# Kernel optimization log

Measured on AMD Instinct MI355X. Metric: run time of the kernel, lower is better.

## Reference

```python
import jax, jax.numpy as jnp
import numpy as np

HIDDEN = 2048
NUM_HEADS = 16
HEAD_DIM = 128
WINDOW_SIZE = 512
NUM_GLOBAL = 16
SCALING = HEAD_DIM ** -0.5


def setup_inputs() -> dict:
    key = jax.random.key(0)
    ks = jax.random.split(key, 5)
    std = HIDDEN ** -0.5
    hidden_states = jax.random.normal(ks[0], (1, 4096, HIDDEN), dtype=jnp.float32)
    # Linear weights stored as (in, out) so y = x @ W
    Wq = jax.random.normal(ks[1], (HIDDEN, NUM_HEADS * HEAD_DIM), dtype=jnp.float32) * std
    Wk = jax.random.normal(ks[2], (HIDDEN, NUM_HEADS * HEAD_DIM), dtype=jnp.float32) * std
    Wv = jax.random.normal(ks[3], (HIDDEN, NUM_HEADS * HEAD_DIM), dtype=jnp.float32) * std
    Wo = jax.random.normal(ks[4], (NUM_HEADS * HEAD_DIM, HIDDEN), dtype=jnp.float32) * std
    return {"hidden_states": hidden_states, "Wq": Wq, "Wk": Wk, "Wv": Wv, "Wo": Wo}


def _sliding_mask(q_len: int, kv_len: int) -> jnp.ndarray:
    q_pos = jnp.arange(q_len)[:, None]
    kv_pos = jnp.arange(kv_len)[None, :]
    half_window = WINDOW_SIZE // 2
    local = jnp.abs(q_pos - kv_pos) < half_window
    glob = (q_pos < NUM_GLOBAL) | (kv_pos < NUM_GLOBAL)
    mask = local | glob
    return jnp.where(mask, 0.0, -jnp.inf).astype(jnp.float32)


def reference(hidden_states, Wq, Wk, Wv, Wo):
    bsz, q_len, _ = hidden_states.shape
    q = (hidden_states @ Wq).reshape(bsz, q_len, NUM_HEADS, HEAD_DIM).transpose(0, 2, 1, 3)
    k = (hidden_states @ Wk).reshape(bsz, q_len, NUM_HEADS, HEAD_DIM).transpose(0, 2, 1, 3)
    v = (hidden_states @ Wv).reshape(bsz, q_len, NUM_HEADS, HEAD_DIM).transpose(0, 2, 1, 3)
    mask = _sliding_mask(q_len, q_len)[None, None]  # [1,1,S,S]
    scores = jnp.einsum("bhqd,bhkd->bhqk", q, k) * SCALING + mask
    attn = jax.nn.softmax(scores.astype(jnp.float32), axis=-1).astype(q.dtype)
    out = jnp.einsum("bhqk,bhkd->bhqd", attn, v)
    out = out.transpose(0, 2, 1, 3).reshape(bsz, q_len, NUM_HEADS * HEAD_DIM)
    return out @ Wo
```

## Files before the change

### kernel.cpp

```cpp
#include <hip/hip_runtime.h>
#include <stdint.h>

#define SEQ    4096
#define HID    2048
#define NQKV   6144
#define NH     16
#define HD     128
#define SCALE  0.08838834764831845f
#define GQC    32

typedef unsigned short u16;
typedef __attribute__((ext_vector_type(8))) short bf16x8;
typedef __attribute__((ext_vector_type(4))) float f32x4;

__device__ __forceinline__ u16 f2bf(float f) {
  union { float f; unsigned u; } v; v.f = f;
  unsigned r = v.u + 0x7FFFu + ((v.u >> 16) & 1u);
  return (u16)(r >> 16);
}

__device__ __forceinline__ float bf2f(u16 b) {
  union { unsigned u; float f; } c; c.u = ((unsigned)b) << 16; return c.f;
}

__device__ __forceinline__ void async16(const u16* g, u16* l) {
  __builtin_amdgcn_global_load_lds(
      (const __attribute__((address_space(1))) unsigned int*)g,
      (__attribute__((address_space(3))) unsigned int*)l, 16, 0, 0);
}

__global__ __launch_bounds__(256) void cvt_f32_bf16(const float* __restrict__ in,
                                                    u16* __restrict__ out, int n4) {
  int i = blockIdx.x * 256 + threadIdx.x;
  if (i >= n4) return;
  float4 v = ((const float4*)in)[i];
  ushort4 o;
  o.x = f2bf(v.x); o.y = f2bf(v.y); o.z = f2bf(v.z); o.w = f2bf(v.w);
  ((ushort4*)out)[i] = o;
}

__global__ __launch_bounds__(256) void transpose_w(const float* __restrict__ W,
                                                   u16* __restrict__ Wt) {
  __shared__ __align__(16) u16 Ts[64 * 72];
  const int n0 = blockIdx.x * 64;
  const int k0 = blockIdx.y * 64;
  const int t = threadIdx.x;
#pragma unroll
  for (int p = 0; p < 4; ++p) {
    int f = (t + p * 256) * 4;
    int r = f >> 6, c = f & 63;
    float4 v = *(const float4*)&W[(size_t)(k0 + r) * 2048 + n0 + c];
    ushort4 o; o.x = f2bf(v.x); o.y = f2bf(v.y); o.z = f2bf(v.z); o.w = f2bf(v.w);
    *(ushort4*)&Ts[r * 72 + c] = o;
  }
  __syncthreads();
#pragma unroll
  for (int p = 0; p < 4; ++p) {
    int g = (t + p * 256) * 4;
    int r = g >> 6, c = g & 63;
    ushort4 o;
    o.x = Ts[(c + 0) * 72 + r];
    o.y = Ts[(c + 1) * 72 + r];
    o.z = Ts[(c + 2) * 72 + r];
    o.w = Ts[(c + 3) * 72 + r];
    *(ushort4*)&Wt[(size_t)(n0 + r) * 2048 + k0 + c] = o;
  }
}

__global__ __launch_bounds__(256) void transpose_v(const u16* __restrict__ qkv,
                                                   u16* __restrict__ vt) {
  __shared__ __align__(16) u16 Ts[64 * 72];
  const int s0 = blockIdx.x * 64;
  const int d0 = blockIdx.y * 64;
  const int h = blockIdx.z;
  const int t = threadIdx.x;
#pragma unroll
  for (int p = 0; p < 2; ++p) {
    int f = (t + p * 256) * 8;
    int r = f >> 6, c = f & 63;
    uint4 v = *(const uint4*)&qkv[(size_t)(s0 + r) * NQKV + 4096 + h * HD + d0 + c];
    *(uint4*)&Ts[r * 72 + c] = v;
  }
  __syncthreads();
#pragma unroll
  for (int p = 0; p < 2; ++p) {
    int g = (t + p * 256) * 8;
    int r = g >> 6, c = g & 63;
    u16 tmp[8];
#pragma unroll
    for (int j = 0; j < 8; ++j) tmp[j] = Ts[(c + j) * 72 + r];
    *(uint4*)&vt[(size_t)h * (HD * SEQ) + (size_t)(d0 + r) * SEQ + s0 + c] = *(uint4*)tmp;
  }
}

template <typename OutT>
__global__ __launch_bounds__(256) void gemm_bt(const u16* __restrict__ A,
                                               const u16* __restrict__ B,
                                               OutT* __restrict__ C,
                                               int K, int ldc) {
  __shared__ __align__(16) u16 As[128 * 32];
  __shared__ __align__(16) u16 Bs[128 * 32];
  const int m0 = blockIdx.y * 128;
  const int n0 = blockIdx.x * 128;
  const int tid = threadIdx.x;
  const int wid = tid >> 6;
  const int lane = tid & 63;
  const int wm = wid & 1, wn = wid >> 1;
  const int l15 = lane & 15, g4 = lane >> 4;

  const int srow = wid * 32 + (lane >> 2);
  const int scol = (lane & 3) * 8;

  f32x4 acc[4][4] = {};

  const u16* pa0 = &A[(size_t)(m0 + srow) * K + scol];
  const u16* pa1 = &A[(size_t)(m0 + srow + 16) * K + scol];
  const u16* pb0 = &B[(size_t)(n0 + srow) * K + scol];
  const u16* pb1 = &B[(size_t)(n0 + srow + 16) * K + scol];
  u16* la0 = &As[(wid * 32) * 32];
  u16* la1 = &As[(wid * 32 + 16) * 32];
  u16* lb0 = &Bs[(wid * 32) * 32];
  u16* lb1 = &Bs[(wid * 32 + 16) * 32];

  for (int kt = 0; kt < K; kt += 32) {
    __syncthreads();
    async16(pa0 + kt, la0);
    async16(pa1 + kt, la1);
    async16(pb0 + kt, lb0);
    async16(pb1 + kt, lb1);
    __syncthreads();
    bf16x8 af[4], bfr[4];
#pragma unroll
    for (int i = 0; i < 4; ++i)
      af[i] = *(const bf16x8*)&As[(wm * 64 + i * 16 + l15) * 32 + g4 * 8];
#pragma unroll
    for (int i = 0; i < 4; ++i)
      bfr[i] = *(const bf16x8*)&Bs[(wn * 64 + i * 16 + l15) * 32 + g4 * 8];
#pragma unroll
    for (int mi = 0; mi < 4; ++mi)
#pragma unroll
      for (int ni = 0; ni < 4; ++ni)
        acc[mi][ni] = __builtin_amdgcn_mfma_f32_16x16x32_bf16(af[mi], bfr[ni], acc[mi][ni], 0, 0, 0);
  }
#pragma unroll
  for (int mi = 0; mi < 4; ++mi)
#pragma unroll
    for (int ni = 0; ni < 4; ++ni) {
      const int n = n0 + wn * 64 + ni * 16 + l15;
#pragma unroll
      for (int r = 0; r < 4; ++r) {
        const int m = m0 + wm * 64 + mi * 16 + g4 * 4 + r;
        float v = acc[mi][ni][r];
        if constexpr (sizeof(OutT) == 2) {
          C[(size_t)m * ldc + n] = (OutT)f2bf(v);
        } else {
          C[(size_t)m * ldc + n] = v;
        }
      }
    }
}

__global__ __launch_bounds__(256) void attn_kernel(const u16* __restrict__ qkv,
                                                   const u16* __restrict__ vt,
                                                   u16* __restrict__ out) {
  __shared__ __align__(16) u16 Qs[64 * 136];
  __shared__ __align__(16) u16 Ks[64 * 136];
  __shared__ __align__(16) u16 VTs[128 * 72];
  __shared__ __align__(16) u16 Ps[64 * 72];
  const int q0 = blockIdx.x * 64;
  const int h = blockIdx.y;
  const int tid = threadIdx.x;
  const int w = tid >> 6;
  const int lane = tid & 63;
  const int l15 = lane & 15, g4 = lane >> 4;

#pragma unroll
  for (int p = 0; p < 4; ++p) {
    int f = (tid + p * 256) * 8;
    int r = f >> 7, c = f & 127;
    uint4 v = *(const uint4*)&qkv[(size_t)(q0 + r) * NQKV + h * HD + c];
    *(uint4*)&Qs[r * 136 + c] = v;
  }

  float m_run = -1e30f, l_run = 0.f;
  f32x4 o[8] = {};

  int lo = q0 - 255;
  int lo_blk = (lo < 0) ? 0 : (lo >> 6);
  int hi_blk = (q0 + 318) >> 6;
  if (hi_blk > 63) hi_blk = 63;
  const int extra = (lo_blk > 0) ? 1 : 0;
  const int nsteps = hi_blk - lo_blk + 1 + extra;

  for (int step = 0; step < nsteps; ++step) {
    const int kb = (extra && step == 0) ? 0 : (lo_blk + step - extra);
    const int kv0 = kb * 64;
    __syncthreads();
#pragma unroll
    for (int p = 0; p < 4; ++p) {
      int f = (tid + p * 256) * 8;
      int r = f >> 7, c = f & 127;
      uint4 v = *(const uint4*)&qkv[(size_t)(kv0 + r) * NQKV + 2048 + h * HD + c];
      *(uint4*)&Ks[r * 136 + c] = v;
    }
#pragma unroll
    for (int p = 0; p < 4; ++p) {
      int f = (tid + p * 256) * 8;
      int r = f >> 6, c = f & 63;
      uint4 v = *(const uint4*)&vt[(size_t)h * (HD * SEQ) + (size_t)r * SEQ + kv0 + c];
      *(uint4*)&VTs[r * 72 + c] = v;
    }
    __syncthreads();

    f32x4 st[4] = {};
#pragma unroll
    for (int kk = 0; kk < 4; ++kk) {
      bf16x8 bq = *(const bf16x8*)&Qs[(w * 16 + l15) * 136 + kk * 32 + g4 * 8];
#pragma unroll
      for (int t4 = 0; t4 < 4; ++t4) {
        bf16x8 ak = *(const bf16x8*)&Ks[(t4 * 16 + l15) * 136 + kk * 32 + g4 * 8];
        st[t4] = __builtin_amdgcn_mfma_f32_16x16x32_bf16(ak, bq, st[t4], 0, 0, 0);
      }
    }

    const int q = q0 + w * 16 + l15;
    float pv[4][4];
    float cmax = -1e30f;
#pragma unroll
    for (int t4 = 0; t4 < 4; ++t4)
#pragma unroll
      for (int r = 0; r < 4; ++r) {
        int kv = kv0 + t4 * 16 + g4 * 4 + r;
        int dq = q - kv; if (dq < 0) dq = -dq;
        bool ok = (dq < 256) || (kv < 16);
        float s = ok ? st[t4][r] * SCALE : -1e30f;
        pv[t4][r] = s;
        cmax = fmaxf(cmax, s);
      }
    cmax = fmaxf(cmax, __shfl_xor(cmax, 16, 64));
    cmax = fmaxf(cmax, __shfl_xor(cmax, 32, 64));
    float mnew = fmaxf(m_run, cmax);
    float csum = 0.f;
#pragma unroll
    for (int t4 = 0; t4 < 4; ++t4)
#pragma unroll
      for (int r = 0; r < 4; ++r) {
        float p = __expf(pv[t4][r] - mnew);
        pv[t4][r] = p;
        csum += p;
      }
    csum += __shfl_xor(csum, 16, 64);
    csum += __shfl_xor(csum, 32, 64);
    float alpha = __expf(m_run - mnew);
    m_run = mnew;
    l_run = l_run * alpha + csum;

#pragma unroll
    for (int t4 = 0; t4 < 4; ++t4) {
      u16 pk[4];
#pragma unroll
      for (int r = 0; r < 4; ++r) pk[r] = f2bf(pv[t4][r]);
      *(uint2*)&Ps[(w * 16 + l15) * 72 + t4 * 16 + g4 * 4] = *(uint2*)pk;
    }

    float al[4];
#pragma unroll
    for (int r = 0; r < 4; ++r) al[r] = __shfl(alpha, g4 * 4 + r, 64);
#pragma unroll
    for (int nt = 0; nt < 8; ++nt)
#pragma unroll
      for (int r = 0; r < 4; ++r) o[nt][r] *= al[r];
    __syncthreads();

#pragma unroll
    for (int ks = 0; ks < 2; ++ks) {
      bf16x8 ap = *(const bf16x8*)&Ps[(w * 16 + l15) * 72 + ks * 32 + g4 * 8];
#pragma unroll
      for (int nt = 0; nt < 8; ++nt) {
        bf16x8 bv = *(const bf16x8*)&VTs[(nt * 16 + l15) * 72 + ks * 32 + g4 * 8];
        o[nt] = __builtin_amdgcn_mfma_f32_16x16x32_bf16(ap, bv, o[nt], 0, 0, 0);
      }
    }
  }

  float lr[4];
#pragma unroll
  for (int r = 0; r < 4; ++r) lr[r] = 1.f / __shfl(l_run, g4 * 4 + r, 64);
#pragma unroll
  for (int nt = 0; nt < 8; ++nt)
#pragma unroll
    for (int r = 0; r < 4; ++r) {
      const int m = q0 + w * 16 + g4 * 4 + r;
      if (m < 16) continue;
      const int n = h * HD + nt * 16 + l15;
      out[(size_t)m * HID + n] = f2bf(o[nt][r] * lr[r]);
    }
}

__global__ __launch_bounds__(256) void attn_global(const u16* __restrict__ qkv,
                                                   float* __restrict__ Opart,
                                                   float* __restrict__ MLpart) {
  __shared__ __align__(16) u16 Ks[64 * 136];
  __shared__ __align__(16) u16 Vs[64 * 136];
  const int chunk = blockIdx.x, h = blockIdx.y;
  const int t = threadIdx.x;
  const int q = t >> 4, dg = t & 15;

  float qr[8];
  {
    bf16x8 v = *(const bf16x8*)&qkv[(size_t)q * NQKV + h * HD + dg * 8];
#pragma unroll
    for (int j = 0; j < 8; ++j) qr[j] = bf2f((u16)v[j]);
  }
  float m_run = -1e30f, l_run = 0.f, o[8] = {};
  const int kvbase = chunk * (SEQ / GQC);

  for (int st = 0; st < (SEQ / GQC) / 64; ++st) {
    const int kv0 = kvbase + st * 64;
    __syncthreads();
#pragma unroll
    for (int p = 0; p < 4; ++p) {
      int f = (t + p * 256) * 8;
      int r = f >> 7, c = f & 127;
      *(uint4*)&Ks[r * 136 + c] = *(const uint4*)&qkv[(size_t)(kv0 + r) * NQKV + 2048 + h * HD + c];
      *(uint4*)&Vs[r * 136 + c] = *(const uint4*)&qkv[(size_t)(kv0 + r) * NQKV + 4096 + h * HD + c];
    }
    __syncthreads();
    for (int kv = 0; kv < 64; ++kv) {
      bf16x8 kr = *(const bf16x8*)&Ks[kv * 136 + dg * 8];
      float s = 0.f;
#pragma unroll
      for (int j = 0; j < 8; ++j) s += qr[j] * bf2f((u16)kr[j]);
      s += __shfl_xor(s, 1, 64); s += __shfl_xor(s, 2, 64);
      s += __shfl_xor(s, 4, 64); s += __shfl_xor(s, 8, 64);
      s *= SCALE;
      float mnew = fmaxf(m_run, s);
      float alpha = __expf(m_run - mnew);
      float p = __expf(s - mnew);
      m_run = mnew;
      l_run = l_run * alpha + p;
      bf16x8 vr = *(const bf16x8*)&Vs[kv * 136 + dg * 8];
#pragma unroll
      for (int j = 0; j < 8; ++j) o[j] = o[j] * alpha + p * bf2f((u16)vr[j]);
    }
  }
  float* op = &Opart[(((size_t)h * GQC + chunk) * 16 + q) * HD + dg * 8];
#pragma unroll
  for (int j = 0; j < 8; ++j) op[j] = o[j];
  if (dg == 0) {
    float* ml = &MLpart[(((size_t)h * GQC + chunk) * 16 + q) * 2];
    ml[0] = m_run; ml[1] = l_run;
  }
}

__global__ __launch_bounds__(256) void attn_gred(const float* __restrict__ Opart,
                                                 const float* __restrict__ MLpart,
                                                 u16* __restrict__ out) {
  const int h = blockIdx.x;
  const int t = threadIdx.x;
  const int q = t >> 4, dg = t & 15;
  float M = -1e30f;
  for (int c = 0; c < GQC; ++c)
    M = fmaxf(M, MLpart[(((size_t)h * GQC + c) * 16 + q) * 2]);
  float L = 0.f, o[8] = {};
  for (int c = 0; c < GQC; ++c) {
    const float* ml = &MLpart[(((size_t)h * GQC + c) * 16 + q) * 2];
    float e = __expf(ml[0] - M);
    L += e * ml[1];
    const float* op = &Opart[(((size_t)h * GQC + c) * 16 + q) * HD + dg * 8];
#pragma unroll
    for (int j = 0; j < 8; ++j) o[j] += e * op[j];
  }
  float inv = 1.f / L;
  u16 tmp[8];
#pragma unroll
  for (int j = 0; j < 8; ++j) tmp[j] = f2bf(o[j] * inv);
  *(uint4*)&out[(size_t)q * HID + h * HD + dg * 8] = *(uint4*)tmp;
}

extern "C" void kernel_launch(void* const* d_in, const int* in_sizes, int n_in,
                              void* d_out, int out_size, void* d_ws, size_t ws_size,
                              hipStream_t stream) {
  const float* X  = (const float*)d_in[0];
  const float* Wq = (const float*)d_in[1];
  const float* Wk = (const float*)d_in[2];
  const float* Wv = (const float*)d_in[3];
  const float* Wo = (const float*)d_in[4];
  float* out = (float*)d_out;

  char* ws = (char*)d_ws;
  u16* Xbf    = (u16*)(ws);
  u16* Wcat   = (u16*)(ws + (size_t)(16 << 20));
  u16* VT     = (u16*)(ws);
  u16* AttnO  = (u16*)(ws + (size_t)(16 << 20));
  float* Opart  = (float*)(ws + (size_t)(32 << 20));
  float* MLpart = (float*)(ws + (size_t)(36 << 20));
  u16* QKV    = (u16*)(ws + (size_t)(40 << 20));
  u16* Wot    = (u16*)(ws + (size_t)(88 << 20));

  cvt_f32_bf16<<<dim3(8192), dim3(256), 0, stream>>>(X, Xbf, (SEQ * HID) / 4);
  dim3 tw(32, 32);
  transpose_w<<<tw, 256, 0, stream>>>(Wq, Wcat);
  transpose_w<<<tw, 256, 0, stream>>>(Wk, Wcat + (size_t)2048 * 2048);
  transpose_w<<<tw, 256, 0, stream>>>(Wv, Wcat + (size_t)2 * 2048 * 2048);
  transpose_w<<<tw, 256, 0, stream>>>(Wo, Wot);
  gemm_bt<u16><<<dim3(48, 32), 256, 0, stream>>>(Xbf, Wcat, QKV, HID, NQKV);
  attn_global<<<dim3(GQC, NH), 256, 0, stream>>>(QKV, Opart, MLpart);
  transpose_v<<<dim3(64, 2, 16), 256, 0, stream>>>(QKV, VT);
  attn_kernel<<<dim3(64, 16), 256, 0, stream>>>(QKV, VT, AttnO);
  attn_gred<<<dim3(NH), 256, 0, stream>>>(Opart, MLpart, AttnO);
  gemm_bt<float><<<dim3(16, 32), 256, 0, stream>>>(AttnO, Wot, out, HID, HID);
}
```

Measured before the change: 452.8 us.

## Swizzle attention LDS tiles, hold Q in registers, merge weight transposes

The attention kernel now keeps Q fragments in registers instead of LDS. K, V^T and P tiles use XOR-swizzled unpadded LDS layouts to avoid bank conflicts, and the launch bounds request 3 blocks per CU. The barrier before the PV MMA is dropped because each wave reads only its own P rows. The four weight transpose launches are merged into one 3D-grid launch to cut launch overhead.

After: 433.2 us. 1.05x faster.

```diff
diff --git a/kernel.cpp b/kernel.cpp
--- a/kernel.cpp
+++ b/kernel.cpp
@@ -39,11 +39,18 @@
   ((ushort4*)out)[i] = o;
 }
 
-__global__ __launch_bounds__(256) void transpose_w(const float* __restrict__ W,
-                                                   u16* __restrict__ Wt) {
+__global__ __launch_bounds__(256) void transpose_w4(const float* __restrict__ W0,
+                                                    const float* __restrict__ W1,
+                                                    const float* __restrict__ W2,
+                                                    const float* __restrict__ W3,
+                                                    u16* __restrict__ Wcat,
+                                                    u16* __restrict__ Wot) {
   __shared__ __align__(16) u16 Ts[64 * 72];
   const int n0 = blockIdx.x * 64;
   const int k0 = blockIdx.y * 64;
+  const int z = blockIdx.z;
+  const float* W = (z == 0) ? W0 : (z == 1) ? W1 : (z == 2) ? W2 : W3;
+  u16* Wt = (z < 3) ? (Wcat + (size_t)z * 2048 * 2048) : Wot;
   const int t = threadIdx.x;
 #pragma unroll
   for (int p = 0; p < 4; ++p) {
@@ -160,26 +167,25 @@
     }
 }
 
-__global__ __launch_bounds__(256) void attn_kernel(const u16* __restrict__ qkv,
-                                                   const u16* __restrict__ vt,
-                                                   u16* __restrict__ out) {
-  __shared__ __align__(16) u16 Qs[64 * 136];
-  __shared__ __align__(16) u16 Ks[64 * 136];
-  __shared__ __align__(16) u16 VTs[128 * 72];
-  __shared__ __align__(16) u16 Ps[64 * 72];
+__global__ __launch_bounds__(256, 3) void attn_kernel(const u16* __restrict__ qkv,
+                                                      const u16* __restrict__ vt,
+                                                      u16* __restrict__ out) {
+  __shared__ __align__(16) u16 Ks[64 * 128];
+  __shared__ __align__(16) u16 VTs[128 * 64];
+  __shared__ __align__(16) u16 Ps[64 * 64];
   const int q0 = blockIdx.x * 64;
   const int h = blockIdx.y;
   const int tid = threadIdx.x;
   const int w = tid >> 6;
   const int lane = tid & 63;
   const int l15 = lane & 15, g4 = lane >> 4;
-
-#pragma unroll
-  for (int p = 0; p < 4; ++p) {
-    int f = (tid + p * 256) * 8;
-    int r = f >> 7, c = f & 127;
-    uint4 v = *(const uint4*)&qkv[(size_t)(q0 + r) * NQKV + h * HD + c];
-    *(uint4*)&Qs[r * 136 + c] = v;
+  const int l7 = l15 & 7;
+
+  bf16x8 qf[4];
+  {
+    const u16* qrow = &qkv[(size_t)(q0 + w * 16 + l15) * NQKV + h * HD + g4 * 8];
+#pragma unroll
+    for (int kk = 0; kk < 4; ++kk) qf[kk] = *(const bf16x8*)&qrow[kk * 32];
   }
 
   float m_run = -1e30f, l_run = 0.f;
@@ -198,28 +204,27 @@
     __syncthreads();
 #pragma unroll
     for (int p = 0; p < 4; ++p) {
-      int f = (tid + p * 256) * 8;
-      int r = f >> 7, c = f & 127;
-      uint4 v = *(const uint4*)&qkv[(size_t)(kv0 + r) * NQKV + 2048 + h * HD + c];
-      *(uint4*)&Ks[r * 136 + c] = v;
+      int id = p * 256 + tid;
+      int r = id >> 4, c8 = id & 15;
+      uint4 v = *(const uint4*)&qkv[(size_t)(kv0 + r) * NQKV + 2048 + h * HD + c8 * 8];
+      *(uint4*)&Ks[r * 128 + ((c8 ^ (r & 15)) * 8)] = v;
     }
 #pragma unroll
     for (int p = 0; p < 4; ++p) {
-      int f = (tid + p * 256) * 8;
-      int r = f >> 6, c = f & 63;
-      uint4 v = *(const uint4*)&vt[(size_t)h * (HD * SEQ) + (size_t)r * SEQ + kv0 + c];
-      *(uint4*)&VTs[r * 72 + c] = v;
+      int id = p * 256 + tid;
+      int r = id >> 3, c8 = id & 7;
+      uint4 v = *(const uint4*)&vt[(size_t)h * (HD * SEQ) + (size_t)r * SEQ + kv0 + c8 * 8];
+      *(uint4*)&VTs[r * 64 + ((c8 ^ (r & 7)) * 8)] = v;
     }
     __syncthreads();
 
     f32x4 st[4] = {};
 #pragma unroll
     for (int kk = 0; kk < 4; ++kk) {
-      bf16x8 bq = *(const bf16x8*)&Qs[(w * 16 + l15) * 136 + kk * 32 + g4 * 8];
 #pragma unroll
       for (int t4 = 0; t4 < 4; ++t4) {
-        bf16x8 ak = *(const bf16x8*)&Ks[(t4 * 16 + l15) * 136 + kk * 32 + g4 * 8];
-        st[t4] = __builtin_amdgcn_mfma_f32_16x16x32_bf16(ak, bq, st[t4], 0, 0, 0);
+        bf16x8 ak = *(const bf16x8*)&Ks[(t4 * 16 + l15) * 128 + (((kk * 4 + g4) ^ l15) * 8)];
+        st[t4] = __builtin_amdgcn_mfma_f32_16x16x32_bf16(ak, qf[kk], st[t4], 0, 0, 0);
       }
     }
 
@@ -260,7 +265,8 @@
       u16 pk[4];
 #pragma unroll
       for (int r = 0; r < 4; ++r) pk[r] = f2bf(pv[t4][r]);
-      *(uint2*)&Ps[(w * 16 + l15) * 72 + t4 * 16 + g4 * 4] = *(uint2*)pk;
+      int c8 = t4 * 2 + (g4 >> 1);
+      *(uint2*)&Ps[(w * 16 + l15) * 64 + ((c8 ^ l7) * 8) + (g4 & 1) * 4] = *(uint2*)pk;
     }
 
     float al[4];
@@ -270,14 +276,13 @@
     for (int nt = 0; nt < 8; ++nt)
 #pragma unroll
       for (int r = 0; r < 4; ++r) o[nt][r] *= al[r];
-    __syncthreads();
 
 #pragma unroll
     for (int ks = 0; ks < 2; ++ks) {
-      bf16x8 ap = *(const bf16x8*)&Ps[(w * 16 + l15) * 72 + ks * 32 + g4 * 8];
+      bf16x8 ap = *(const bf16x8*)&Ps[(w * 16 + l15) * 64 + (((ks * 4 + g4) ^ l7) * 8)];
 #pragma unroll
       for (int nt = 0; nt < 8; ++nt) {
-        bf16x8 bv = *(const bf16x8*)&VTs[(nt * 16 + l15) * 72 + ks * 32 + g4 * 8];
+        bf16x8 bv = *(const bf16x8*)&VTs[(nt * 16 + l15) * 64 + (((ks * 4 + g4) ^ l7) * 8)];
         o[nt] = __builtin_amdgcn_mfma_f32_16x16x32_bf16(ap, bv, o[nt], 0, 0, 0);
       }
     }
@@ -399,11 +404,7 @@
   u16* Wot    = (u16*)(ws + (size_t)(88 << 20));
 
   cvt_f32_bf16<<<dim3(8192), dim3(256), 0, stream>>>(X, Xbf, (SEQ * HID) / 4);
-  dim3 tw(32, 32);
-  transpose_w<<<tw, 256, 0, stream>>>(Wq, Wcat);
-  transpose_w<<<tw, 256, 0, stream>>>(Wk, Wcat + (size_t)2048 * 2048);
-  transpose_w<<<tw, 256, 0, stream>>>(Wv, Wcat + (size_t)2 * 2048 * 2048);
-  transpose_w<<<tw, 256, 0, stream>>>(Wo, Wot);
+  transpose_w4<<<dim3(32, 32, 4), 256, 0, stream>>>(Wq, Wk, Wv, Wo, Wcat, Wot);
   gemm_bt<u16><<<dim3(48, 32), 256, 0, stream>>>(Xbf, Wcat, QKV, HID, NQKV);
   attn_global<<<dim3(GQC, NH), 256, 0, stream>>>(QKV, Opart, MLpart);
   transpose_v<<<dim3(64, 2, 16), 256, 0, stream>>>(QKV, VT);
```
